# Optimization experiments

Hardware: AMD Instinct MI355X
Metric: run time of the kernel (lower is better)

The kernel has to match this reference:

```python
import jax, jax.numpy as jnp
import numpy as np

B, S, D, H = 2, 4096, 512, 8
DH = D // H  # head dim = 64

def setup_inputs() -> dict:
    key = jax.random.key(0)
    ks = jax.random.split(key, 9)
    s = 0.02
    return {
        "Q": jax.random.normal(ks[0], (B, S, D), jnp.float32),
        "Wq": jax.random.normal(ks[1], (D, D), jnp.float32) * s,
        "bq": jnp.zeros((D,), jnp.float32),
        "Wk": jax.random.normal(ks[2], (D, D), jnp.float32) * s,
        "bk": jnp.zeros((D,), jnp.float32),
        "Wv": jax.random.normal(ks[3], (D, D), jnp.float32) * s,
        "bv": jnp.zeros((D,), jnp.float32),
        "Wo": jax.random.normal(ks[4], (D, D), jnp.float32) * s,
        "bo": jnp.zeros((D,), jnp.float32),
    }

def reference(Q, Wq, bq, Wk, bk, Wv, bv, Wo, bo):
    bs, s, d = Q.shape
    scale = DH ** -0.5
    # torch Linear: x @ W.T + b, W is [out, in]
    q = (Q @ Wq.T + bq).reshape(bs, s, H, DH).transpose(0, 2, 1, 3)  # [b,h,s,dh]
    k = (Q @ Wk.T + bk).reshape(bs, s, H, DH).transpose(0, 2, 1, 3)
    v = (Q @ Wv.T + bv).reshape(bs, s, H, DH).transpose(0, 2, 1, 3)
    scores = jnp.einsum('bhqd,bhkd->bhqk', q, k) * scale  # [b,h,s,s]
    attn = jax.nn.softmax(scores, axis=-1)
    out = jnp.einsum('bhqk,bhkd->bhqd', attn, v)  # [b,h,s,dh]
    out = out.transpose(0, 2, 1, 3).reshape(bs, s, H * DH)
    out = out @ Wo.T + bo
    return (out, attn)
```

## Files before the change

kernel.cpp:

```cpp
#include <hip/hip_runtime.h>
#include <hip/hip_bf16.h>

#define B_  2
#define S_  4096
#define D_  512
#define H_  8
#define DH_ 64
#define BH_ 16
#define M_  (B_*S_)

typedef __attribute__((ext_vector_type(4))) float f32x4;
typedef __attribute__((ext_vector_type(8))) short s16x8;
typedef __attribute__((ext_vector_type(4))) short s16x4;

#define MFMA(A,Bv,C) __builtin_amdgcn_mfma_f32_16x16x32_bf16(A,Bv,C,0,0,0)

typedef const void __attribute__((address_space(1)))* gas_t;
typedef void __attribute__((address_space(3)))* las_t;
#define GLDS(gp, lp) __builtin_amdgcn_global_load_lds((gas_t)(gp), (las_t)(lp), 16, 0, 0)

#define EXP_C 0.18033688011112042f

static __device__ __forceinline__ unsigned short f2bf(float f){
    union { __hip_bfloat16 h; unsigned short u; } v;
    v.h = __float2bfloat16(f);
    return v.u;
}
static __device__ __forceinline__ float bf2f(unsigned short b){
    union { unsigned int u; float f; } v; v.u = ((unsigned int)b) << 16;
    return v.f;
}

__global__ __launch_bounds__(256) void cvt_all(const float* __restrict__ Q,
                                               const float* __restrict__ W0, const float* __restrict__ W1,
                                               const float* __restrict__ W2, const float* __restrict__ W3,
                                               unsigned short* __restrict__ Qd,
                                               unsigned short* __restrict__ D0, unsigned short* __restrict__ D1,
                                               unsigned short* __restrict__ D2, unsigned short* __restrict__ D3){
    int i = blockIdx.x * 256 + threadIdx.x;
    const float* s; unsigned short* d; int off;
    if (i < 1048576){ s = Q; d = Qd; off = i; }
    else {
        int j = i - 1048576;
        int w = j >> 16; off = j & 65535;
        s = (w==0)?W0:(w==1)?W1:(w==2)?W2:W3;
        d = (w==0)?D0:(w==1)?D1:(w==2)?D2:D3;
    }
    float4 v = reinterpret_cast<const float4*>(s)[off];
    ushort4 o;
    o.x = f2bf(v.x); o.y = f2bf(v.y); o.z = f2bf(v.z); o.w = f2bf(v.w);
    reinterpret_cast<ushort4*>(d)[off] = o;
}

__global__ __launch_bounds__(256) void gemm_qkv(const unsigned short* __restrict__ A,
                                                const unsigned short* __restrict__ Wq, const float* __restrict__ bq,
                                                const unsigned short* __restrict__ Wk, const float* __restrict__ bk,
                                                const unsigned short* __restrict__ Wv, const float* __restrict__ bv,
                                                unsigned short* __restrict__ qh, unsigned short* __restrict__ kh,
                                                unsigned short* __restrict__ vT){
    __shared__ unsigned short tile[64][65];
    const int mt = blockIdx.x, nt0 = blockIdx.y;
    const int wave = threadIdx.x >> 6, lane = threadIdx.x & 63;
    const int g = lane >> 4, r16 = lane & 15;
    const unsigned short* Ap = A + (size_t)(mt*64 + wave*16 + r16) * 512;
    const int b  = mt >> 6;
    const int s0 = (mt & 63) * 64;
    const int h  = nt0;

    #pragma unroll 1
    for (int w = 0; w < 3; ++w){
        const unsigned short* W = (w==0)?Wq:(w==1)?Wk:Wv;
        const float* bias       = (w==0)?bq:(w==1)?bk:bv;

        f32x4 acc[4];
        #pragma unroll
        for (int i = 0; i < 4; ++i) acc[i] = (f32x4){0.f,0.f,0.f,0.f};

        #pragma unroll
        for (int k0 = 0; k0 < 512; k0 += 64){
            s16x8 a0 = *(const s16x8*)(Ap + k0 + g*8);
            s16x8 a1 = *(const s16x8*)(Ap + k0 + 32 + g*8);
            #pragma unroll
            for (int nt = 0; nt < 4; ++nt){
                const unsigned short* Wp = W + (size_t)(nt0*64 + nt*16 + r16)*512 + k0 + g*8;
                s16x8 b0 = *(const s16x8*)(Wp);
                s16x8 b1 = *(const s16x8*)(Wp + 32);
                acc[nt] = MFMA(a0, b0, acc[nt]);
                acc[nt] = MFMA(a1, b1, acc[nt]);
            }
        }

        if (w < 2){
            unsigned short* dst = (w==0) ? qh : kh;
            #pragma unroll
            for (int nt = 0; nt < 4; ++nt){
                const float bv_ = bias[nt0*64 + nt*16 + r16];
                #pragma unroll
                for (int r = 0; r < 4; ++r){
                    const int s = s0 + wave*16 + g*4 + r;
                    dst[((size_t)(b*H_ + h)*S_ + s)*DH_ + nt*16 + r16] = f2bf(acc[nt][r] + bv_);
                }
            }
        } else {
            #pragma unroll
            for (int nt = 0; nt < 4; ++nt){
                const float bv_ = bias[nt0*64 + nt*16 + r16];
                #pragma unroll
                for (int r = 0; r < 4; ++r)
                    tile[wave*16 + g*4 + r][nt*16 + r16] = f2bf(acc[nt][r] + bv_);
            }
            __syncthreads();
            const int c = threadIdx.x & 63, r4 = threadIdx.x >> 6;
            unsigned short* dst = vT + (size_t)(b*H_ + h)*DH_*S_;
            #pragma unroll
            for (int i = 0; i < 16; ++i){
                const int dh = i*4 + r4;
                dst[(size_t)dh*S_ + s0 + c] = tile[c][dh];
            }
        }
    }
}

__global__ __launch_bounds__(256) void gemm_bt(const unsigned short* __restrict__ A,
                                               const unsigned short* __restrict__ W,
                                               const float* __restrict__ bias,
                                               float* __restrict__ dst){
    const int mt = blockIdx.x, nt0 = blockIdx.y;
    const int wave = threadIdx.x >> 6, lane = threadIdx.x & 63;
    const int g = lane >> 4, r16 = lane & 15;
    const unsigned short* Ap = A + (size_t)(mt*64 + wave*16 + r16) * 512;

    f32x4 acc[4];
    #pragma unroll
    for (int i = 0; i < 4; ++i) acc[i] = (f32x4){0.f,0.f,0.f,0.f};

    #pragma unroll
    for (int k0 = 0; k0 < 512; k0 += 64){
        s16x8 a0 = *(const s16x8*)(Ap + k0 + g*8);
        s16x8 a1 = *(const s16x8*)(Ap + k0 + 32 + g*8);
        #pragma unroll
        for (int nt = 0; nt < 4; ++nt){
            const unsigned short* Wp = W + (size_t)(nt0*64 + nt*16 + r16)*512 + k0 + g*8;
            s16x8 b0 = *(const s16x8*)(Wp);
            s16x8 b1 = *(const s16x8*)(Wp + 32);
            acc[nt] = MFMA(a0, b0, acc[nt]);
            acc[nt] = MFMA(a1, b1, acc[nt]);
        }
    }

    #pragma unroll
    for (int nt = 0; nt < 4; ++nt){
        const float bv = bias[nt0*64 + nt*16 + r16];
        #pragma unroll
        for (int r = 0; r < 4; ++r){
            const int orow = mt*64 + wave*16 + g*4 + r;
            dst[(size_t)orow*512 + nt0*64 + nt*16 + r16] = acc[nt][r] + bv;
        }
    }
}

__global__ __launch_bounds__(512, 4) void attn_fused(const unsigned short* __restrict__ qh,
                                                     const unsigned short* __restrict__ kh,
                                                     const unsigned short* __restrict__ vT,
                                                     float* __restrict__ attn,
                                                     unsigned short* __restrict__ ctx){
    __shared__ unsigned short Kb[3*64*64];
    __shared__ unsigned short Vb[2][64][64];
    __shared__ __align__(16) unsigned short Pbf[8][16][136];

    const int lin = blockIdx.y * 32 + blockIdx.x;
    const int nl  = (lin & 7) * 64 + (lin >> 3);
    const int qt  = nl & 31;
    const int bh  = nl >> 5;

    const int wave = threadIdx.x >> 6, lane = threadIdx.x & 63;
    const int g = lane >> 4, r16 = lane & 15;

    const unsigned short* qbase = qh + (size_t)bh*S_*DH_;
    const unsigned short* kbase = kh + (size_t)bh*S_*DH_;
    const unsigned short* vbase = vT + (size_t)bh*DH_*S_;

    const int tr = wave*8 + (lane >> 3);
    const int cc = (lane & 7) ^ (tr & 7);
    const int stg = tr*64 + (lane & 7)*8;

    const int sw = r16 & 7;
    const int c0 = (g ^ sw) * 8;
    const int c1 = ((4 + g) ^ sw) * 8;

    const int qrow = qt*128 + wave*16 + r16;
    s16x8 qa0 = *(const s16x8*)(qbase + (size_t)qrow*DH_ + g*8);
    s16x8 qa1 = *(const s16x8*)(qbase + (size_t)qrow*DH_ + 32 + g*8);

    GLDS(kbase + (size_t)tr*DH_ + cc*8,          Kb + 0*4096 + stg);
    GLDS(kbase + (size_t)(64 + tr)*DH_ + cc*8,   Kb + 1*4096 + stg);

    float lsum[4] = {0.f,0.f,0.f,0.f};
    for (int t = 0; t < 64; ++t){
        if (t == 63) asm volatile("s_waitcnt vmcnt(0)" ::: "memory");
        else         asm volatile("s_waitcnt vmcnt(1)" ::: "memory");
        __builtin_amdgcn_s_barrier();
        __builtin_amdgcn_sched_barrier(0);
        if (t < 62){
            const int s2 = (t + 2) % 3;
            GLDS(kbase + (size_t)((t+2)*64 + tr)*DH_ + cc*8, Kb + s2*4096 + stg);
        }
        __builtin_amdgcn_sched_barrier(0);
        const unsigned short* Kt = Kb + (t % 3)*4096;
        #pragma unroll
        for (int nt = 0; nt < 4; ++nt){
            const int row = nt*16 + r16;
            s16x8 b0 = *(const s16x8*)(Kt + row*64 + c0);
            s16x8 b1 = *(const s16x8*)(Kt + row*64 + c1);
            f32x4 acc = (f32x4){0.f,0.f,0.f,0.f};
            acc = MFMA(qa0, b0, acc);
            acc = MFMA(qa1, b1, acc);
            #pragma unroll
            for (int r = 0; r < 4; ++r)
                lsum[r] += __builtin_amdgcn_exp2f(acc[r]*EXP_C);
        }
    }

    #pragma unroll
    for (int m = 1; m < 16; m <<= 1){
        #pragma unroll
        for (int r = 0; r < 4; ++r) lsum[r] += __shfl_xor(lsum[r], m, 64);
    }
    float inv[4];
    #pragma unroll
    for (int r = 0; r < 4; ++r) inv[r] = 1.0f / lsum[r];

    __builtin_amdgcn_s_barrier();
    __builtin_amdgcn_sched_barrier(0);
    GLDS(kbase + (size_t)tr*DH_ + cc*8, Kb + 0*4096 + stg);
    GLDS(vbase + (size_t)tr*S_  + cc*8, &Vb[0][0][0] + stg);
    asm volatile("s_waitcnt vmcnt(0)" ::: "memory");
    __builtin_amdgcn_s_barrier();
    __builtin_amdgcn_sched_barrier(0);

    f32x4 oacc[4];
    #pragma unroll
    for (int i = 0; i < 4; ++i) oacc[i] = (f32x4){0.f,0.f,0.f,0.f};

    float* attnW = attn + ((size_t)bh*S_ + qt*128 + wave*16)*S_;
    unsigned short (*Pw)[136] = Pbf[wave];
    const int sl = lane & 31, sh = lane >> 5;

    auto compute_tile = [&](int t){
        const unsigned short* Kt = Kb + (t&1)*4096;
        const unsigned short (*Vt)[64] = Vb[t&1];
        const int cb = (t&1)*64;
        f32x4 pacc[4];
        #pragma unroll
        for (int nt = 0; nt < 4; ++nt){
            const int row = nt*16 + r16;
            s16x8 b0 = *(const s16x8*)(Kt + row*64 + c0);
            s16x8 b1 = *(const s16x8*)(Kt + row*64 + c1);
            f32x4 acc = (f32x4){0.f,0.f,0.f,0.f};
            acc = MFMA(qa0, b0, acc);
            acc = MFMA(qa1, b1, acc);
            pacc[nt] = acc;
        }
        #pragma unroll
        for (int nt = 0; nt < 4; ++nt){
            #pragma unroll
            for (int r = 0; r < 4; ++r){
                float p = __builtin_amdgcn_exp2f(pacc[nt][r]*EXP_C) * inv[r];
                Pw[g*4 + r][cb + nt*16 + r16] = f2bf(p);
            }
        }
        s16x8 pa0 = *(const s16x8*)(&Pw[r16][cb + g*8]);
        s16x8 pa1 = *(const s16x8*)(&Pw[r16][cb + 32 + g*8]);
        #pragma unroll
        for (int nt = 0; nt < 4; ++nt){
            const int row = nt*16 + r16;
            s16x8 v0 = *(const s16x8*)(&Vt[row][c0]);
            s16x8 v1 = *(const s16x8*)(&Vt[row][c1]);
            oacc[nt] = MFMA(pa0, v0, oacc[nt]);
            oacc[nt] = MFMA(pa1, v1, oacc[nt]);
        }
    };

    auto store_pair = [&](int tfirst){
        #pragma unroll
        for (int i = 0; i < 8; ++i){
            const int row = i*2 + sh;
            s16x4 pb = *(const s16x4*)(&Pw[row][sl*4]);
            f32x4 o;
            #pragma unroll
            for (int j = 0; j < 4; ++j) o[j] = bf2f((unsigned short)pb[j]);
            __builtin_nontemporal_store(o,
                (f32x4*)(attnW + (size_t)row*S_ + tfirst*64 + sl*4));
        }
    };

    GLDS(kbase + (size_t)(1*64 + tr)*DH_ + cc*8, Kb + 1*4096 + stg);
    GLDS(vbase + (size_t)tr*S_ + 1*64 + cc*8,    &Vb[1][0][0] + stg);
    __builtin_amdgcn_sched_barrier(0);
    compute_tile(0);
    asm volatile("s_waitcnt vmcnt(0)" ::: "memory");
    __builtin_amdgcn_s_barrier();
    __builtin_amdgcn_sched_barrier(0);

    for (int t = 1; t < 64; ++t){
        const int nxt = (t + 1) & 63;
        GLDS(kbase + (size_t)(nxt*64 + tr)*DH_ + cc*8, Kb + ((t&1)^1)*4096 + stg);
        GLDS(vbase + (size_t)tr*S_ + nxt*64 + cc*8,    &Vb[(t&1)^1][0][0] + stg);
        __builtin_amdgcn_sched_barrier(0);
        if ((t & 1) == 0){
            store_pair(t - 2);
            __builtin_amdgcn_sched_barrier(0);
        }
        compute_tile(t);
        if (t & 1){
            asm volatile("s_waitcnt vmcnt(0)" ::: "memory");
        } else {
            asm volatile("s_waitcnt vmcnt(8)" ::: "memory");
        }
        __builtin_amdgcn_s_barrier();
        __builtin_amdgcn_sched_barrier(0);
    }
    store_pair(62);

    const int b = bh >> 3, h = bh & 7;
    #pragma unroll
    for (int nt = 0; nt < 4; ++nt){
        #pragma unroll
        for (int r = 0; r < 4; ++r){
            const int qr = qt*128 + wave*16 + g*4 + r;
            ctx[(size_t)(b*S_ + qr)*D_ + h*64 + nt*16 + r16] = f2bf(oacc[nt][r]);
        }
    }
}

extern "C" void kernel_launch(void* const* d_in, const int* in_sizes, int n_in,
                              void* d_out, int out_size, void* d_ws, size_t ws_size,
                              hipStream_t stream){
    const float* Q  = (const float*)d_in[0];
    const float* Wq = (const float*)d_in[1];
    const float* bq = (const float*)d_in[2];
    const float* Wk = (const float*)d_in[3];
    const float* bk = (const float*)d_in[4];
    const float* Wv = (const float*)d_in[5];
    const float* bv = (const float*)d_in[6];
    const float* Wo = (const float*)d_in[7];
    const float* bo = (const float*)d_in[8];

    float* out  = (float*)d_out;
    float* attn = out + (size_t)M_*D_;

    unsigned short* Qbf = (unsigned short*)attn;
    unsigned short* Wqb = Qbf + (size_t)M_*D_;
    unsigned short* Wkb = Wqb + 512*512;
    unsigned short* Wvb = Wkb + 512*512;

    unsigned short* qhb = (unsigned short*)d_ws;
    unsigned short* khb = qhb + (size_t)BH_*S_*DH_;
    unsigned short* vTb = khb + (size_t)BH_*S_*DH_;
    unsigned short* ctx = vTb + (size_t)BH_*S_*DH_;
    unsigned short* Wob = ctx + (size_t)M_*D_;

    cvt_all<<<dim3(5120), 256, 0, stream>>>(Q, Wq, Wk, Wv, Wo, Qbf, Wqb, Wkb, Wvb, Wob);

    gemm_qkv<<<dim3(M_/64, 8), 256, 0, stream>>>(Qbf, Wqb, bq, Wkb, bk, Wvb, bv,
                                                 qhb, khb, vTb);

    attn_fused<<<dim3(32, BH_), 512, 0, stream>>>(qhb, khb, vTb, attn, ctx);

    gemm_bt<<<dim3(M_/64, D_/64), 256, 0, stream>>>(ctx, Wob, bo, out);
}
```

Measured before the change: 377.3 us.

## Fuse Q fp32-to-bf16 conversion into QKV GEMM and enlarge GEMM tiles

Removes the separate bf16 conversion pass over the activation Q: the QKV GEMM now loads fp32 rows directly, converts them in registers, and keeps the whole A row slice resident across the three weight matrices. Both projection GEMMs move to 512-thread blocks covering 128 rows, with A held in registers instead of reloaded per k-step. The weight conversion becomes a small 2D-grid kernel. This cuts one full read/write pass over Q and some weight reloads, at the cost of more registers per thread and fewer blocks.

```diff
diff --git a/kernel.cpp b/kernel.cpp
--- a/kernel.cpp
+++ b/kernel.cpp
@@ -31,41 +31,55 @@
     return v.f;
 }
 
-__global__ __launch_bounds__(256) void cvt_all(const float* __restrict__ Q,
-                                               const float* __restrict__ W0, const float* __restrict__ W1,
-                                               const float* __restrict__ W2, const float* __restrict__ W3,
-                                               unsigned short* __restrict__ Qd,
-                                               unsigned short* __restrict__ D0, unsigned short* __restrict__ D1,
-                                               unsigned short* __restrict__ D2, unsigned short* __restrict__ D3){
+__global__ __launch_bounds__(256) void cvt_w4(const float* __restrict__ s0, const float* __restrict__ s1,
+                                              const float* __restrict__ s2, const float* __restrict__ s3,
+                                              unsigned short* __restrict__ d0, unsigned short* __restrict__ d1,
+                                              unsigned short* __restrict__ d2, unsigned short* __restrict__ d3){
+    const float* s; unsigned short* d;
+    switch (blockIdx.y){
+        case 0: s = s0; d = d0; break;
+        case 1: s = s1; d = d1; break;
+        case 2: s = s2; d = d2; break;
+        default: s = s3; d = d3; break;
+    }
     int i = blockIdx.x * 256 + threadIdx.x;
-    const float* s; unsigned short* d; int off;
-    if (i < 1048576){ s = Q; d = Qd; off = i; }
-    else {
-        int j = i - 1048576;
-        int w = j >> 16; off = j & 65535;
-        s = (w==0)?W0:(w==1)?W1:(w==2)?W2:W3;
-        d = (w==0)?D0:(w==1)?D1:(w==2)?D2:D3;
-    }
-    float4 v = reinterpret_cast<const float4*>(s)[off];
+    float4 v = reinterpret_cast<const float4*>(s)[i];
     ushort4 o;
     o.x = f2bf(v.x); o.y = f2bf(v.y); o.z = f2bf(v.z); o.w = f2bf(v.w);
-    reinterpret_cast<ushort4*>(d)[off] = o;
-}
-
-__global__ __launch_bounds__(256) void gemm_qkv(const unsigned short* __restrict__ A,
-                                                const unsigned short* __restrict__ Wq, const float* __restrict__ bq,
-                                                const unsigned short* __restrict__ Wk, const float* __restrict__ bk,
-                                                const unsigned short* __restrict__ Wv, const float* __restrict__ bv,
-                                                unsigned short* __restrict__ qh, unsigned short* __restrict__ kh,
-                                                unsigned short* __restrict__ vT){
-    __shared__ unsigned short tile[64][65];
-    const int mt = blockIdx.x, nt0 = blockIdx.y;
+    reinterpret_cast<ushort4*>(d)[i] = o;
+}
+
+__global__ __launch_bounds__(512, 4) void gemm_qkv(const float* __restrict__ Q,
+                                                   const unsigned short* __restrict__ Wq, const float* __restrict__ bq,
+                                                   const unsigned short* __restrict__ Wk, const float* __restrict__ bk,
+                                                   const unsigned short* __restrict__ Wv, const float* __restrict__ bv,
+                                                   unsigned short* __restrict__ qh, unsigned short* __restrict__ kh,
+                                                   unsigned short* __restrict__ vT){
+    __shared__ unsigned short tile[128][65];
+    const int mt = blockIdx.x, h = blockIdx.y;
     const int wave = threadIdx.x >> 6, lane = threadIdx.x & 63;
     const int g = lane >> 4, r16 = lane & 15;
-    const unsigned short* Ap = A + (size_t)(mt*64 + wave*16 + r16) * 512;
-    const int b  = mt >> 6;
-    const int s0 = (mt & 63) * 64;
-    const int h  = nt0;
+    const int b  = mt >> 5;
+    const int s0 = (mt & 31) * 128;
+
+    s16x8 areg[16];
+    {
+        const float* Arow = Q + (size_t)(mt*128 + wave*16 + r16) * 512;
+        #pragma unroll
+        for (int j = 0; j < 8; ++j){
+            float4 l0 = *(const float4*)(Arow + j*64 + g*8);
+            float4 l1 = *(const float4*)(Arow + j*64 + g*8 + 4);
+            float4 h0 = *(const float4*)(Arow + j*64 + 32 + g*8);
+            float4 h1 = *(const float4*)(Arow + j*64 + 32 + g*8 + 4);
+            union { s16x8 v; unsigned short u[8]; } t0, t1;
+            t0.u[0]=f2bf(l0.x); t0.u[1]=f2bf(l0.y); t0.u[2]=f2bf(l0.z); t0.u[3]=f2bf(l0.w);
+            t0.u[4]=f2bf(l1.x); t0.u[5]=f2bf(l1.y); t0.u[6]=f2bf(l1.z); t0.u[7]=f2bf(l1.w);
+            t1.u[0]=f2bf(h0.x); t1.u[1]=f2bf(h0.y); t1.u[2]=f2bf(h0.z); t1.u[3]=f2bf(h0.w);
+            t1.u[4]=f2bf(h1.x); t1.u[5]=f2bf(h1.y); t1.u[6]=f2bf(h1.z); t1.u[7]=f2bf(h1.w);
+            areg[2*j]   = t0.v;
+            areg[2*j+1] = t1.v;
+        }
+    }
 
     #pragma unroll 1
     for (int w = 0; w < 3; ++w){
@@ -77,16 +91,14 @@
         for (int i = 0; i < 4; ++i) acc[i] = (f32x4){0.f,0.f,0.f,0.f};
 
         #pragma unroll
-        for (int k0 = 0; k0 < 512; k0 += 64){
-            s16x8 a0 = *(const s16x8*)(Ap + k0 + g*8);
-            s16x8 a1 = *(const s16x8*)(Ap + k0 + 32 + g*8);
+        for (int j = 0; j < 8; ++j){
             #pragma unroll
             for (int nt = 0; nt < 4; ++nt){
-                const unsigned short* Wp = W + (size_t)(nt0*64 + nt*16 + r16)*512 + k0 + g*8;
+                const unsigned short* Wp = W + (size_t)(h*64 + nt*16 + r16)*512 + j*64 + g*8;
                 s16x8 b0 = *(const s16x8*)(Wp);
                 s16x8 b1 = *(const s16x8*)(Wp + 32);
-                acc[nt] = MFMA(a0, b0, acc[nt]);
-                acc[nt] = MFMA(a1, b1, acc[nt]);
+                acc[nt] = MFMA(areg[2*j],   b0, acc[nt]);
+                acc[nt] = MFMA(areg[2*j+1], b1, acc[nt]);
             }
         }
 
@@ -94,7 +106,7 @@
             unsigned short* dst = (w==0) ? qh : kh;
             #pragma unroll
             for (int nt = 0; nt < 4; ++nt){
-                const float bv_ = bias[nt0*64 + nt*16 + r16];
+                const float bv_ = bias[h*64 + nt*16 + r16];
                 #pragma unroll
                 for (int r = 0; r < 4; ++r){
                     const int s = s0 + wave*16 + g*4 + r;
@@ -104,13 +116,13 @@
         } else {
             #pragma unroll
             for (int nt = 0; nt < 4; ++nt){
-                const float bv_ = bias[nt0*64 + nt*16 + r16];
+                const float bv_ = bias[h*64 + nt*16 + r16];
                 #pragma unroll
                 for (int r = 0; r < 4; ++r)
                     tile[wave*16 + g*4 + r][nt*16 + r16] = f2bf(acc[nt][r] + bv_);
             }
             __syncthreads();
-            const int c = threadIdx.x & 63, r4 = threadIdx.x >> 6;
+            const int c = threadIdx.x & 127, r4 = threadIdx.x >> 7;
             unsigned short* dst = vT + (size_t)(b*H_ + h)*DH_*S_;
             #pragma unroll
             for (int i = 0; i < 16; ++i){
@@ -121,30 +133,37 @@
     }
 }
 
-__global__ __launch_bounds__(256) void gemm_bt(const unsigned short* __restrict__ A,
-                                               const unsigned short* __restrict__ W,
-                                               const float* __restrict__ bias,
-                                               float* __restrict__ dst){
+__global__ __launch_bounds__(512, 4) void gemm_o(const unsigned short* __restrict__ A,
+                                                 const unsigned short* __restrict__ W,
+                                                 const float* __restrict__ bias,
+                                                 float* __restrict__ dst){
     const int mt = blockIdx.x, nt0 = blockIdx.y;
     const int wave = threadIdx.x >> 6, lane = threadIdx.x & 63;
     const int g = lane >> 4, r16 = lane & 15;
-    const unsigned short* Ap = A + (size_t)(mt*64 + wave*16 + r16) * 512;
+
+    s16x8 areg[16];
+    {
+        const unsigned short* Arow = A + (size_t)(mt*128 + wave*16 + r16) * 512;
+        #pragma unroll
+        for (int j = 0; j < 8; ++j){
+            areg[2*j]   = *(const s16x8*)(Arow + j*64 + g*8);
+            areg[2*j+1] = *(const s16x8*)(Arow + j*64 + 32 + g*8);
+        }
+    }
 
     f32x4 acc[4];
     #pragma unroll
     for (int i = 0; i < 4; ++i) acc[i] = (f32x4){0.f,0.f,0.f,0.f};
 
     #pragma unroll
-    for (int k0 = 0; k0 < 512; k0 += 64){
-        s16x8 a0 = *(const s16x8*)(Ap + k0 + g*8);
-        s16x8 a1 = *(const s16x8*)(Ap + k0 + 32 + g*8);
-        #pragma unroll
-        for (int nt = 0; nt < 4; ++nt){
-            const unsigned short* Wp = W + (size_t)(nt0*64 + nt*16 + r16)*512 + k0 + g*8;
+    for (int j = 0; j < 8; ++j){
+        #pragma unroll
+        for (int nt = 0; nt < 4; ++nt){
+            const unsigned short* Wp = W + (size_t)(nt0*64 + nt*16 + r16)*512 + j*64 + g*8;
             s16x8 b0 = *(const s16x8*)(Wp);
             s16x8 b1 = *(const s16x8*)(Wp + 32);
-            acc[nt] = MFMA(a0, b0, acc[nt]);
-            acc[nt] = MFMA(a1, b1, acc[nt]);
+            acc[nt] = MFMA(areg[2*j],   b0, acc[nt]);
+            acc[nt] = MFMA(areg[2*j+1], b1, acc[nt]);
         }
     }
 
@@ -153,7 +172,7 @@
         const float bv = bias[nt0*64 + nt*16 + r16];
         #pragma unroll
         for (int r = 0; r < 4; ++r){
-            const int orow = mt*64 + wave*16 + g*4 + r;
+            const int orow = mt*128 + wave*16 + g*4 + r;
             dst[(size_t)orow*512 + nt0*64 + nt*16 + r16] = acc[nt][r] + bv;
         }
     }
@@ -349,8 +368,7 @@
     float* out  = (float*)d_out;
     float* attn = out + (size_t)M_*D_;
 
-    unsigned short* Qbf = (unsigned short*)attn;
-    unsigned short* Wqb = Qbf + (size_t)M_*D_;
+    unsigned short* Wqb = (unsigned short*)attn;
     unsigned short* Wkb = Wqb + 512*512;
     unsigned short* Wvb = Wkb + 512*512;
 
@@ -360,12 +378,12 @@
     unsigned short* ctx = vTb + (size_t)BH_*S_*DH_;
     unsigned short* Wob = ctx + (size_t)M_*D_;
 
-    cvt_all<<<dim3(5120), 256, 0, stream>>>(Q, Wq, Wk, Wv, Wo, Qbf, Wqb, Wkb, Wvb, Wob);
-
-    gemm_qkv<<<dim3(M_/64, 8), 256, 0, stream>>>(Qbf, Wqb, bq, Wkb, bk, Wvb, bv,
-                                                 qhb, khb, vTb);
+    cvt_w4<<<dim3(256, 4), 256, 0, stream>>>(Wq, Wk, Wv, Wo, Wqb, Wkb, Wvb, Wob);
+
+    gemm_qkv<<<dim3(M_/128, 8), 512, 0, stream>>>(Q, Wqb, bq, Wkb, bk, Wvb, bv,
+                                                  qhb, khb, vTb);
 
     attn_fused<<<dim3(32, BH_), 512, 0, stream>>>(qhb, khb, vTb, attn, ctx);
 
-    gemm_bt<<<dim3(M_/64, D_/64), 256, 0, stream>>>(ctx, Wob, bo, out);
-}
+    gemm_o<<<dim3(M_/128, D_/64), 512, 0, stream>>>(ctx, Wob, bo, out);
+}
```

Result: slower. 389.1 us (+3.1%).
